# Optimization experiments

Measured on AMD Instinct MI355X. Metric: run time of the kernel, lower is better.

## Reference

```python
import jax, jax.numpy as jnp
import numpy as np

IOU_THRESHOLD = 0.1
EPS = 1e-7  # torchvision generalized_box_iou_loss eps


def _make_boxes(key, b, n, img=1000.0, wmin=10.0, wmax=120.0):
    k1, k2 = jax.random.split(key)
    cxy = jax.random.uniform(k1, (b, n, 2), jnp.float32, 0.0, img)
    wh = jax.random.uniform(k2, (b, n, 2), jnp.float32, wmin, wmax)
    return jnp.concatenate([cxy - 0.5 * wh, cxy + 0.5 * wh], axis=-1)  # xyxy


def setup_inputs() -> dict:
    key = jax.random.key(0)
    kp, kt = jax.random.split(key)
    pred_boxes = _make_boxes(kp, 16, 4096)    # [B, M, 4]
    target_boxes = _make_boxes(kt, 16, 512)   # [B, N, 4]
    return {"pred_boxes": pred_boxes, "target_boxes": target_boxes}


def _pairwise_iou(p, t):
    # p: [M,4], t: [N,4] xyxy -> [M,N]
    area_p = (p[:, 2] - p[:, 0]) * (p[:, 3] - p[:, 1])
    area_t = (t[:, 2] - t[:, 0]) * (t[:, 3] - t[:, 1])
    lt = jnp.maximum(p[:, None, :2], t[None, :, :2])
    rb = jnp.minimum(p[:, None, 2:], t[None, :, 2:])
    wh = jnp.clip(rb - lt, 0.0)
    inter = wh[..., 0] * wh[..., 1]
    union = area_p[:, None] + area_t[None, :] - inter
    return inter / union


def _greedy_match(iou):
    # Greedy: for each pred row (in order), take highest-IoU unused target with IoU > thr.
    N = iou.shape[1]
    def step(used, row):
        masked = jnp.where(used, -jnp.inf, row)  # [N]
        j = jnp.argmax(masked)
        valid = masked[j] > IOU_THRESHOLD
        used = used.at[j].set(used[j] | valid)
        return used, (j, valid)
    _, (idx, valid) = jax.lax.scan(step, jnp.zeros((N,), bool), iou)
    return idx, valid  # [M] int, [M] bool


def _giou_loss_pairs(p, t):
    # elementwise GIoU loss between p[i] and t[i]; p,t: [K,4] -> [K]
    x1 = jnp.maximum(p[:, 0], t[:, 0]); y1 = jnp.maximum(p[:, 1], t[:, 1])
    x2 = jnp.minimum(p[:, 2], t[:, 2]); y2 = jnp.minimum(p[:, 3], t[:, 3])
    inter = jnp.clip(x2 - x1, 0.0) * jnp.clip(y2 - y1, 0.0)
    area_p = (p[:, 2] - p[:, 0]) * (p[:, 3] - p[:, 1])
    area_t = (t[:, 2] - t[:, 0]) * (t[:, 3] - t[:, 1])
    union = area_p + area_t - inter
    iou = inter / (union + EPS)
    ex1 = jnp.minimum(p[:, 0], t[:, 0]); ey1 = jnp.minimum(p[:, 1], t[:, 1])
    ex2 = jnp.maximum(p[:, 2], t[:, 2]); ey2 = jnp.maximum(p[:, 3], t[:, 3])
    enc = (ex2 - ex1) * (ey2 - ey1)
    giou = iou - (enc - union) / (enc + EPS)
    return 1.0 - giou


def _image_loss(pred, tgt):
    # pred [M,4], tgt [N,4] with M != N -> greedy match then mean GIoU loss over matches
    iou = _pairwise_iou(pred, tgt)
    idx, valid = _greedy_match(iou)
    matched_t = tgt[idx]                    # [M,4]
    loss = _giou_loss_pairs(pred, matched_t)
    w = valid.astype(loss.dtype)
    cnt = w.sum()
    return jnp.where(cnt > 0, (loss * w).sum() / jnp.maximum(cnt, 1.0), 0.0)


def reference(pred_boxes, target_boxes):
    # batched path, reduction='mean': mean over per-image mean GIoU losses
    per_image = jax.vmap(_image_loss)(pred_boxes, target_boxes)  # [B]
    return per_image.mean()
```

## Files before the change

### kernel.cpp

```cpp
#include <hip/hip_runtime.h>
#include <math.h>

#define NB   16
#define NM   4096
#define NT   512
#define CAP  16
#define IOU_THR 0.1f
#define EPSG 1e-7f
#define NROWS (NB*NM)
#define T_WIN 1024
#define WROWS 2048
#define NWIN  (NM / WROWS)
#define SENT  0xFFFFFFFFu

__global__ __launch_bounds__(256) void cand_kernel(
    const float4* __restrict__ pred, const float4* __restrict__ tgt,
    int* __restrict__ counts, float2* __restrict__ cands, int* __restrict__ done_ctr)
{
    __shared__ float4 t_lds[NT];
    const int rb = blockIdx.x * 32;
    const int b  = rb >> 12;
    if (blockIdx.x == 0 && threadIdx.x == 0) *done_ctr = 0;
    #pragma unroll
    for (int i = 0; i < 2; ++i)
        t_lds[i * 256 + threadIdx.x] = tgt[b * NT + i * 256 + threadIdx.x];
    __syncthreads();

    const int wv = threadIdx.x >> 6, lane = threadIdx.x & 63;
    const int row0 = rb + wv * 8;
    const unsigned long long lmask = (1ull << lane) - 1ull;

    float4 pn0 = pred[row0],     pn1 = pred[row0 + 1];
    float4 pn2 = pred[row0 + 2], pn3 = pred[row0 + 3];
    for (int rr = 0; rr < 8; rr += 4) {
        float4 p0 = pn0, p1 = pn1, p2 = pn2, p3 = pn3;
        if (rr + 4 < 8) {
            pn0 = pred[row0 + rr + 4]; pn1 = pred[row0 + rr + 5];
            pn2 = pred[row0 + rr + 6]; pn3 = pred[row0 + rr + 7];
        }
        float ap0 = (p0.z - p0.x) * (p0.w - p0.y);
        float ap1 = (p1.z - p1.x) * (p1.w - p1.y);
        float ap2 = (p2.z - p2.x) * (p2.w - p2.y);
        float ap3 = (p3.z - p3.x) * (p3.w - p3.y);
        int base0 = 0, base1 = 0, base2 = 0, base3 = 0;
        #pragma unroll
        for (int pass = 0; pass < NT / 64; ++pass) {
            int j = (pass << 6) + lane;
            float4 t = t_lds[j];
            float at = (t.z - t.x) * (t.w - t.y);
            float w0 = fmaxf(fminf(p0.z, t.z) - fmaxf(p0.x, t.x), 0.f);
            float h0 = fmaxf(fminf(p0.w, t.w) - fmaxf(p0.y, t.y), 0.f);
            float in0 = w0 * h0;
            float iou0 = in0 * __builtin_amdgcn_rcpf((ap0 + at) - in0);
            float w1 = fmaxf(fminf(p1.z, t.z) - fmaxf(p1.x, t.x), 0.f);
            float h1 = fmaxf(fminf(p1.w, t.w) - fmaxf(p1.y, t.y), 0.f);
            float in1 = w1 * h1;
            float iou1 = in1 * __builtin_amdgcn_rcpf((ap1 + at) - in1);
            float w2 = fmaxf(fminf(p2.z, t.z) - fmaxf(p2.x, t.x), 0.f);
            float h2 = fmaxf(fminf(p2.w, t.w) - fmaxf(p2.y, t.y), 0.f);
            float in2 = w2 * h2;
            float iou2 = in2 * __builtin_amdgcn_rcpf((ap2 + at) - in2);
            float w3 = fmaxf(fminf(p3.z, t.z) - fmaxf(p3.x, t.x), 0.f);
            float h3 = fmaxf(fminf(p3.w, t.w) - fmaxf(p3.y, t.y), 0.f);
            float in3 = w3 * h3;
            float iou3 = in3 * __builtin_amdgcn_rcpf((ap3 + at) - in3);
            bool q0 = iou0 > IOU_THR, q1 = iou1 > IOU_THR;
            bool q2 = iou2 > IOU_THR, q3 = iou3 > IOU_THR;
            unsigned long long m0 = __ballot(q0), m1 = __ballot(q1);
            unsigned long long m2 = __ballot(q2), m3 = __ballot(q3);
            if (q0) {
                int off = base0 + __popcll(m0 & lmask);
                if (off < CAP)
                    cands[(size_t)off * NROWS + row0 + rr]     = make_float2(iou0, __int_as_float(j));
            }
            if (q1) {
                int off = base1 + __popcll(m1 & lmask);
                if (off < CAP)
                    cands[(size_t)off * NROWS + row0 + rr + 1] = make_float2(iou1, __int_as_float(j));
            }
            if (q2) {
                int off = base2 + __popcll(m2 & lmask);
                if (off < CAP)
                    cands[(size_t)off * NROWS + row0 + rr + 2] = make_float2(iou2, __int_as_float(j));
            }
            if (q3) {
                int off = base3 + __popcll(m3 & lmask);
                if (off < CAP)
                    cands[(size_t)off * NROWS + row0 + rr + 3] = make_float2(iou3, __int_as_float(j));
            }
            base0 += __popcll(m0); base1 += __popcll(m1);
            base2 += __popcll(m2); base3 += __popcll(m3);
        }
        if (lane == 0) {
            counts[row0 + rr]     = base0;
            counts[row0 + rr + 1] = base1;
            counts[row0 + rr + 2] = base2;
            counts[row0 + rr + 3] = base3;
        }
    }
}

__global__ __launch_bounds__(T_WIN) void win_auction(
    const float4* __restrict__ pred, const float4* __restrict__ tgt,
    const int* __restrict__ counts, const float2* __restrict__ cands,
    float* __restrict__ per_img, int* __restrict__ done_ctr,
    float* __restrict__ out)
{
    __shared__ float4   t_lds[NT];
    __shared__ unsigned claim[NT];
    __shared__ int lastprop;
    __shared__ unsigned char winovf[NWIN];
    __shared__ int ovf_min, ovf_res;
    __shared__ float rvv[T_WIN / 64];  __shared__ int rjj[T_WIN / 64];
    __shared__ float rls[T_WIN / 64];  __shared__ float rcs[T_WIN / 64];

    const int b = blockIdx.x, t = threadIdx.x, gbase = b * NM;
    const int wv = t >> 6, lane = t & 63;

    if (t < NT) {
        t_lds[t] = tgt[b * NT + t];
        claim[t] = SENT;
    }
    if (t < NWIN) winovf[t] = 0;
    if (t == 0) lastprop = -1;
    __syncthreads();

    int cw00, cw01, cw10, cw11;
    cw00 = counts[gbase + 0 * WROWS + t];
    cw01 = counts[gbase + 0 * WROWS + T_WIN + t];
    cw10 = counts[gbase + 1 * WROWS + t];
    cw11 = counts[gbase + 1 * WROWS + T_WIN + t];
    if (cw00 > CAP || cw01 > CAP) winovf[0] = 1;
    if (cw10 > CAP || cw11 > CAP) winovf[1] = 1;
    __syncthreads();

    int rglob = 0;
    #pragma unroll 1
    for (int w = 0; w < NWIN; ++w) {
        float2 c0[CAP], c1[CAP];
        #pragma unroll
        for (int e = 0; e < CAP; ++e) {
            c0[e] = cands[(size_t)e * NROWS + gbase + w * WROWS + t];
            c1[e] = cands[(size_t)e * NROWS + gbase + w * WROWS + T_WIN + t];
        }
        const unsigned row0 = (unsigned)(w * WROWS + t);
        const unsigned row1 = (unsigned)(w * WROWS + T_WIN + t);
        const int cnt0 = (w == 0) ? cw00 : cw10;
        const int cnt1 = (w == 0) ? cw01 : cw11;
        int  stt0 = (cnt0 > 0 && cnt0 <= CAP) ? 0 : 2;
        int  stt1 = (cnt1 > 0 && cnt1 <= CAP) ? 0 : 2;
        int  myj0 = -1, myj1 = -1;
        bool isovf0 = (cnt0 > CAP), isovf1 = (cnt1 > CAP);
        int  ovfj0 = -1, ovfj1 = -1;

        for (;;) {
            for (;;) {
                bool did = false;
                if (stt0 == 1 && claim[myj0] != row0) stt0 = 0;
                if (stt0 == 0) {
                    for (int it = 0; it <= CAP; ++it) {
                        float bv = -1.f; int bj = -1;
                        #pragma unroll
                        for (int e = 0; e < CAP; ++e) {
                            float2 ce = c0[e];
                            int j = __float_as_int(ce.y) & (NT - 1);
                            unsigned cj = claim[j];
                            if (e < cnt0 && cj >= row0 && ce.x > bv) { bv = ce.x; bj = j; }
                        }
                        if (bj < 0) { stt0 = 2; break; }
                        did = true;
                        unsigned old = atomicMin(&claim[bj], row0);
                        if (old >= row0) { myj0 = bj; stt0 = 1; break; }
                    }
                }
                if (stt1 == 1 && claim[myj1] != row1) stt1 = 0;
                if (stt1 == 0) {
                    for (int it = 0; it <= CAP; ++it) {
                        float bv = -1.f; int bj = -1;
                        #pragma unroll
                        for (int e = 0; e < CAP; ++e) {
                            float2 ce = c1[e];
                            int j = __float_as_int(ce.y) & (NT - 1);
                            unsigned cj = claim[j];
                            if (e < cnt1 && cj >= row1 && ce.x > bv) { bv = ce.x; bj = j; }
                        }
                        if (bj < 0) { stt1 = 2; break; }
                        did = true;
                        unsigned old = atomicMin(&claim[bj], row1);
                        if (old >= row1) { myj1 = bj; stt1 = 1; break; }
                    }
                }
                if (did) lastprop = rglob;
                __syncthreads();
                int lp = lastprop;
                ++rglob;
                if (lp < rglob - 1) break;
            }
            if (!winovf[w]) break;
            if (t == 0) ovf_min = 0x7FFFFFFF;
            __syncthreads();
            bool pend0 = isovf0 && (ovfj0 < 0 || claim[ovfj0] != row0);
            bool pend1 = isovf1 && (ovfj1 < 0 || claim[ovfj1] != row1);
            if (pend0) atomicMin(&ovf_min, (int)row0);
            if (pend1) atomicMin(&ovf_min, (int)row1);
            __syncthreads();
            const int rowF = ovf_min;
            if (rowF == 0x7FFFFFFF) break;
            {
                float4 p4 = pred[gbase + rowF];
                float v = -1.f; int bj = NT;
                if (t < NT) {
                    float4 tt = t_lds[t];
                    float area_p = (p4.z - p4.x) * (p4.w - p4.y);
                    float area_t = (tt.z - tt.x) * (tt.w - tt.y);
                    float wd = fmaxf(fminf(p4.z, tt.z) - fmaxf(p4.x, tt.x), 0.f);
                    float hd = fmaxf(fminf(p4.w, tt.w) - fmaxf(p4.y, tt.y), 0.f);
                    float inter = wd * hd;
                    float iou = inter / ((area_p + area_t) - inter);
                    bool freej = claim[t] > (unsigned)rowF;
                    v = freej ? iou : -1.f;
                    bj = freej ? t : NT;
                }
                #pragma unroll
                for (int off = 1; off < 64; off <<= 1) {
                    float ov = __shfl_xor(v, off);
                    int   oj = __shfl_xor(bj, off);
                    if (ov > v || (ov == v && oj < bj)) { v = ov; bj = oj; }
                }
                if (lane == 0) { rvv[wv] = v; rjj[wv] = bj; }
            }
            __syncthreads();
            if (t == 0) {
                float v = rvv[0]; int bj = rjj[0];
                for (int q = 1; q < T_WIN / 64; ++q)
                    if (rvv[q] > v || (rvv[q] == v && rjj[q] < bj)) { v = rvv[q]; bj = rjj[q]; }
                if (v > IOU_THR) { ovf_res = bj; claim[bj] = (unsigned)rowF; }
                else ovf_res = -1;
            }
            __syncthreads();
            if ((int)row0 == rowF) {
                if (ovf_res >= 0) ovfj0 = ovf_res;
                else isovf0 = false;
            }
            if ((int)row1 == rowF) {
                if (ovf_res >= 0) ovfj1 = ovf_res;
                else isovf1 = false;
            }
        }
    }
    __syncthreads();

    float ls = 0.f, cs = 0.f;
    if (t < NT) {
        unsigned r = claim[t];
        if (r != SENT) {
            float4 p4 = pred[gbase + (int)r];
            float4 tt = t_lds[t];
            float inter = fmaxf(fminf(p4.z, tt.z) - fmaxf(p4.x, tt.x), 0.f) *
                          fmaxf(fminf(p4.w, tt.w) - fmaxf(p4.y, tt.y), 0.f);
            float area_p = (p4.z - p4.x) * (p4.w - p4.y);
            float area_t = (tt.z - tt.x) * (tt.w - tt.y);
            float uni = area_p + area_t - inter;
            float iou = inter / (uni + EPSG);
            float enc = (fmaxf(p4.z, tt.z) - fminf(p4.x, tt.x)) *
                        (fmaxf(p4.w, tt.w) - fminf(p4.y, tt.y));
            float giou = iou - (enc - uni) / (enc + EPSG);
            ls = 1.f - giou;
            cs = 1.f;
        }
    }
    #pragma unroll
    for (int off = 32; off >= 1; off >>= 1) {
        ls += __shfl_xor(ls, off);
        cs += __shfl_xor(cs, off);
    }
    if (lane == 0) { rls[wv] = ls; rcs[wv] = cs; }
    __syncthreads();
    if (t == 0) {
        float L = 0.f, C = 0.f;
        for (int q = 0; q < T_WIN / 64; ++q) { L += rls[q]; C += rcs[q]; }
        per_img[b] = (C > 0.f) ? L / C : 0.f;
        __threadfence();
        int ret = atomicAdd(done_ctr, 1);
        if (ret == NB - 1) {
            __threadfence();
            volatile float* vp = per_img;
            float s = 0.f;
            for (int i = 0; i < NB; ++i) s += vp[i];
            out[0] = s / (float)NB;
        }
    }
}

extern "C" void kernel_launch(void* const* d_in, const int* in_sizes, int n_in,
                              void* d_out, int out_size, void* d_ws, size_t ws_size,
                              hipStream_t stream)
{
    const float4* pred = (const float4*)d_in[0];
    const float4* tgt  = (const float4*)d_in[1];

    char* ws = (char*)d_ws;
    int*    counts  = (int*)ws;
    size_t  off1    = (size_t)NROWS * sizeof(int);
    float2* cands   = (float2*)(ws + off1);
    size_t  off2    = off1 + (size_t)CAP * NROWS * sizeof(float2);
    float*  per_img = (float*)(ws + off2);
    int*    done_ctr = (int*)(ws + off2 + 64);

    cand_kernel<<<NROWS / 32, 256, 0, stream>>>(pred, tgt, counts, cands, done_ctr);
    win_auction<<<NB, T_WIN, 0, stream>>>(pred, tgt, counts, cands, per_img,
                                          done_ctr, (float*)d_out);
}
```

Measured before the change: 54.38 us.

## Fuse candidate and auction kernels with producer-consumer window flags

Merges the candidate-generation kernel and the per-image auction kernel into one launch. The first 16 blocks run the auction, and 512 producer blocks of 1024 threads compute candidates and bump per-window atomic counters that the auction blocks spin on. The aim is to overlap the auction on window 0 with candidate generation for later rows and to remove the gap between two launches. It adds a memset, spin-waiting, and a dependency on the auction blocks being resident alongside the producers; block scheduling order matters for forward progress.

```diff
diff --git a/kernel.cpp b/kernel.cpp
--- a/kernel.cpp
+++ b/kernel.cpp
@@ -8,145 +8,145 @@
 #define IOU_THR 0.1f
 #define EPSG 1e-7f
 #define NROWS (NB*NM)
-#define T_WIN 1024
+#define T_BLK 1024
 #define WROWS 2048
 #define NWIN  (NM / WROWS)
+#define NPROD 512
 #define SENT  0xFFFFFFFFu
 
-__global__ __launch_bounds__(256) void cand_kernel(
+__global__ __launch_bounds__(T_BLK) void fused_kernel(
     const float4* __restrict__ pred, const float4* __restrict__ tgt,
-    int* __restrict__ counts, float2* __restrict__ cands, int* __restrict__ done_ctr)
-{
-    __shared__ float4 t_lds[NT];
-    const int rb = blockIdx.x * 32;
-    const int b  = rb >> 12;
-    if (blockIdx.x == 0 && threadIdx.x == 0) *done_ctr = 0;
-    #pragma unroll
-    for (int i = 0; i < 2; ++i)
-        t_lds[i * 256 + threadIdx.x] = tgt[b * NT + i * 256 + threadIdx.x];
-    __syncthreads();
-
-    const int wv = threadIdx.x >> 6, lane = threadIdx.x & 63;
-    const int row0 = rb + wv * 8;
-    const unsigned long long lmask = (1ull << lane) - 1ull;
-
-    float4 pn0 = pred[row0],     pn1 = pred[row0 + 1];
-    float4 pn2 = pred[row0 + 2], pn3 = pred[row0 + 3];
-    for (int rr = 0; rr < 8; rr += 4) {
-        float4 p0 = pn0, p1 = pn1, p2 = pn2, p3 = pn3;
-        if (rr + 4 < 8) {
-            pn0 = pred[row0 + rr + 4]; pn1 = pred[row0 + rr + 5];
-            pn2 = pred[row0 + rr + 6]; pn3 = pred[row0 + rr + 7];
-        }
-        float ap0 = (p0.z - p0.x) * (p0.w - p0.y);
-        float ap1 = (p1.z - p1.x) * (p1.w - p1.y);
-        float ap2 = (p2.z - p2.x) * (p2.w - p2.y);
-        float ap3 = (p3.z - p3.x) * (p3.w - p3.y);
-        int base0 = 0, base1 = 0, base2 = 0, base3 = 0;
-        #pragma unroll
-        for (int pass = 0; pass < NT / 64; ++pass) {
-            int j = (pass << 6) + lane;
-            float4 t = t_lds[j];
-            float at = (t.z - t.x) * (t.w - t.y);
-            float w0 = fmaxf(fminf(p0.z, t.z) - fmaxf(p0.x, t.x), 0.f);
-            float h0 = fmaxf(fminf(p0.w, t.w) - fmaxf(p0.y, t.y), 0.f);
-            float in0 = w0 * h0;
-            float iou0 = in0 * __builtin_amdgcn_rcpf((ap0 + at) - in0);
-            float w1 = fmaxf(fminf(p1.z, t.z) - fmaxf(p1.x, t.x), 0.f);
-            float h1 = fmaxf(fminf(p1.w, t.w) - fmaxf(p1.y, t.y), 0.f);
-            float in1 = w1 * h1;
-            float iou1 = in1 * __builtin_amdgcn_rcpf((ap1 + at) - in1);
-            float w2 = fmaxf(fminf(p2.z, t.z) - fmaxf(p2.x, t.x), 0.f);
-            float h2 = fmaxf(fminf(p2.w, t.w) - fmaxf(p2.y, t.y), 0.f);
-            float in2 = w2 * h2;
-            float iou2 = in2 * __builtin_amdgcn_rcpf((ap2 + at) - in2);
-            float w3 = fmaxf(fminf(p3.z, t.z) - fmaxf(p3.x, t.x), 0.f);
-            float h3 = fmaxf(fminf(p3.w, t.w) - fmaxf(p3.y, t.y), 0.f);
-            float in3 = w3 * h3;
-            float iou3 = in3 * __builtin_amdgcn_rcpf((ap3 + at) - in3);
-            bool q0 = iou0 > IOU_THR, q1 = iou1 > IOU_THR;
-            bool q2 = iou2 > IOU_THR, q3 = iou3 > IOU_THR;
-            unsigned long long m0 = __ballot(q0), m1 = __ballot(q1);
-            unsigned long long m2 = __ballot(q2), m3 = __ballot(q3);
-            if (q0) {
-                int off = base0 + __popcll(m0 & lmask);
-                if (off < CAP)
-                    cands[(size_t)off * NROWS + row0 + rr]     = make_float2(iou0, __int_as_float(j));
-            }
-            if (q1) {
-                int off = base1 + __popcll(m1 & lmask);
-                if (off < CAP)
-                    cands[(size_t)off * NROWS + row0 + rr + 1] = make_float2(iou1, __int_as_float(j));
-            }
-            if (q2) {
-                int off = base2 + __popcll(m2 & lmask);
-                if (off < CAP)
-                    cands[(size_t)off * NROWS + row0 + rr + 2] = make_float2(iou2, __int_as_float(j));
-            }
-            if (q3) {
-                int off = base3 + __popcll(m3 & lmask);
-                if (off < CAP)
-                    cands[(size_t)off * NROWS + row0 + rr + 3] = make_float2(iou3, __int_as_float(j));
-            }
-            base0 += __popcll(m0); base1 += __popcll(m1);
-            base2 += __popcll(m2); base3 += __popcll(m3);
-        }
-        if (lane == 0) {
-            counts[row0 + rr]     = base0;
-            counts[row0 + rr + 1] = base1;
-            counts[row0 + rr + 2] = base2;
-            counts[row0 + rr + 3] = base3;
-        }
-    }
-}
-
-__global__ __launch_bounds__(T_WIN) void win_auction(
-    const float4* __restrict__ pred, const float4* __restrict__ tgt,
-    const int* __restrict__ counts, const float2* __restrict__ cands,
-    float* __restrict__ per_img, int* __restrict__ done_ctr,
-    float* __restrict__ out)
+    int* __restrict__ counts, float2* __restrict__ cands,
+    int* __restrict__ prod_win, float* __restrict__ per_img,
+    int* __restrict__ done_ctr, float* __restrict__ out)
 {
     __shared__ float4   t_lds[NT];
     __shared__ unsigned claim[NT];
     __shared__ int lastprop;
-    __shared__ unsigned char winovf[NWIN];
     __shared__ int ovf_min, ovf_res;
-    __shared__ float rvv[T_WIN / 64];  __shared__ int rjj[T_WIN / 64];
-    __shared__ float rls[T_WIN / 64];  __shared__ float rcs[T_WIN / 64];
-
-    const int b = blockIdx.x, t = threadIdx.x, gbase = b * NM;
+    __shared__ float rvv[T_BLK / 64];  __shared__ int rjj[T_BLK / 64];
+    __shared__ float rls[T_BLK / 64];  __shared__ float rcs[T_BLK / 64];
+
+    const int blk = blockIdx.x, t = threadIdx.x;
     const int wv = t >> 6, lane = t & 63;
 
+    if (blk >= NB) {
+        const int q  = blk - NB;
+        const int rb = q * 128;
+        const int b  = rb >> 12;
+        if (t < NT) t_lds[t] = tgt[b * NT + t];
+        __syncthreads();
+
+        const int row0 = rb + wv * 8;
+        const unsigned long long lmask = (1ull << lane) - 1ull;
+
+        float4 pn0 = pred[row0],     pn1 = pred[row0 + 1];
+        float4 pn2 = pred[row0 + 2], pn3 = pred[row0 + 3];
+        for (int rr = 0; rr < 8; rr += 4) {
+            float4 p0 = pn0, p1 = pn1, p2 = pn2, p3 = pn3;
+            if (rr + 4 < 8) {
+                pn0 = pred[row0 + rr + 4]; pn1 = pred[row0 + rr + 5];
+                pn2 = pred[row0 + rr + 6]; pn3 = pred[row0 + rr + 7];
+            }
+            float ap0 = (p0.z - p0.x) * (p0.w - p0.y);
+            float ap1 = (p1.z - p1.x) * (p1.w - p1.y);
+            float ap2 = (p2.z - p2.x) * (p2.w - p2.y);
+            float ap3 = (p3.z - p3.x) * (p3.w - p3.y);
+            int base0 = 0, base1 = 0, base2 = 0, base3 = 0;
+            #pragma unroll
+            for (int pass = 0; pass < NT / 64; ++pass) {
+                int j = (pass << 6) + lane;
+                float4 tb = t_lds[j];
+                float at = (tb.z - tb.x) * (tb.w - tb.y);
+                float w0 = fmaxf(fminf(p0.z, tb.z) - fmaxf(p0.x, tb.x), 0.f);
+                float h0 = fmaxf(fminf(p0.w, tb.w) - fmaxf(p0.y, tb.y), 0.f);
+                float in0 = w0 * h0;
+                float iou0 = in0 * __builtin_amdgcn_rcpf((ap0 + at) - in0);
+                float w1 = fmaxf(fminf(p1.z, tb.z) - fmaxf(p1.x, tb.x), 0.f);
+                float h1 = fmaxf(fminf(p1.w, tb.w) - fmaxf(p1.y, tb.y), 0.f);
+                float in1 = w1 * h1;
+                float iou1 = in1 * __builtin_amdgcn_rcpf((ap1 + at) - in1);
+                float w2 = fmaxf(fminf(p2.z, tb.z) - fmaxf(p2.x, tb.x), 0.f);
+                float h2 = fmaxf(fminf(p2.w, tb.w) - fmaxf(p2.y, tb.y), 0.f);
+                float in2 = w2 * h2;
+                float iou2 = in2 * __builtin_amdgcn_rcpf((ap2 + at) - in2);
+                float w3 = fmaxf(fminf(p3.z, tb.z) - fmaxf(p3.x, tb.x), 0.f);
+                float h3 = fmaxf(fminf(p3.w, tb.w) - fmaxf(p3.y, tb.y), 0.f);
+                float in3 = w3 * h3;
+                float iou3 = in3 * __builtin_amdgcn_rcpf((ap3 + at) - in3);
+                bool q0 = iou0 > IOU_THR, q1 = iou1 > IOU_THR;
+                bool q2 = iou2 > IOU_THR, q3 = iou3 > IOU_THR;
+                unsigned long long m0 = __ballot(q0), m1 = __ballot(q1);
+                unsigned long long m2 = __ballot(q2), m3 = __ballot(q3);
+                if (q0) {
+                    int off = base0 + __popcll(m0 & lmask);
+                    if (off < CAP)
+                        cands[(size_t)off * NROWS + row0 + rr]     = make_float2(iou0, __int_as_float(j));
+                }
+                if (q1) {
+                    int off = base1 + __popcll(m1 & lmask);
+                    if (off < CAP)
+                        cands[(size_t)off * NROWS + row0 + rr + 1] = make_float2(iou1, __int_as_float(j));
+                }
+                if (q2) {
+                    int off = base2 + __popcll(m2 & lmask);
+                    if (off < CAP)
+                        cands[(size_t)off * NROWS + row0 + rr + 2] = make_float2(iou2, __int_as_float(j));
+                }
+                if (q3) {
+                    int off = base3 + __popcll(m3 & lmask);
+                    if (off < CAP)
+                        cands[(size_t)off * NROWS + row0 + rr + 3] = make_float2(iou3, __int_as_float(j));
+                }
+                base0 += __popcll(m0); base1 += __popcll(m1);
+                base2 += __popcll(m2); base3 += __popcll(m3);
+            }
+            if (lane == 0) {
+                counts[row0 + rr]     = base0;
+                counts[row0 + rr + 1] = base1;
+                counts[row0 + rr + 2] = base2;
+                counts[row0 + rr + 3] = base3;
+            }
+        }
+        __syncthreads();
+        if (t == 0) {
+            __threadfence();
+            atomicAdd(&prod_win[q >> 4], 1);
+        }
+        return;
+    }
+
+    const int b = blk, gbase = b * NM;
     if (t < NT) {
         t_lds[t] = tgt[b * NT + t];
         claim[t] = SENT;
     }
-    if (t < NWIN) winovf[t] = 0;
     if (t == 0) lastprop = -1;
-    __syncthreads();
-
-    int cw00, cw01, cw10, cw11;
-    cw00 = counts[gbase + 0 * WROWS + t];
-    cw01 = counts[gbase + 0 * WROWS + T_WIN + t];
-    cw10 = counts[gbase + 1 * WROWS + t];
-    cw11 = counts[gbase + 1 * WROWS + T_WIN + t];
-    if (cw00 > CAP || cw01 > CAP) winovf[0] = 1;
-    if (cw10 > CAP || cw11 > CAP) winovf[1] = 1;
     __syncthreads();
 
     int rglob = 0;
     #pragma unroll 1
     for (int w = 0; w < NWIN; ++w) {
+        if (t == 0) {
+            while (__hip_atomic_load(&prod_win[b * 2 + w], __ATOMIC_ACQUIRE,
+                                     __HIP_MEMORY_SCOPE_AGENT) < 16) {}
+            __threadfence();
+        }
+        __syncthreads();
+
+        const int cnt0 = counts[gbase + w * WROWS + t];
+        const int cnt1 = counts[gbase + w * WROWS + T_BLK + t];
+        int novf = __syncthreads_count(cnt0 > CAP || cnt1 > CAP);
+        const bool haveovf = (novf > 0);
+
         float2 c0[CAP], c1[CAP];
         #pragma unroll
         for (int e = 0; e < CAP; ++e) {
             c0[e] = cands[(size_t)e * NROWS + gbase + w * WROWS + t];
-            c1[e] = cands[(size_t)e * NROWS + gbase + w * WROWS + T_WIN + t];
+            c1[e] = cands[(size_t)e * NROWS + gbase + w * WROWS + T_BLK + t];
         }
         const unsigned row0 = (unsigned)(w * WROWS + t);
-        const unsigned row1 = (unsigned)(w * WROWS + T_WIN + t);
-        const int cnt0 = (w == 0) ? cw00 : cw10;
-        const int cnt1 = (w == 0) ? cw01 : cw11;
+        const unsigned row1 = (unsigned)(w * WROWS + T_BLK + t);
         int  stt0 = (cnt0 > 0 && cnt0 <= CAP) ? 0 : 2;
         int  stt1 = (cnt1 > 0 && cnt1 <= CAP) ? 0 : 2;
         int  myj0 = -1, myj1 = -1;
@@ -196,7 +196,7 @@
                 ++rglob;
                 if (lp < rglob - 1) break;
             }
-            if (!winovf[w]) break;
+            if (!haveovf) break;
             if (t == 0) ovf_min = 0x7FFFFFFF;
             __syncthreads();
             bool pend0 = isovf0 && (ovfj0 < 0 || claim[ovfj0] != row0);
@@ -232,8 +232,8 @@
             __syncthreads();
             if (t == 0) {
                 float v = rvv[0]; int bj = rjj[0];
-                for (int q = 1; q < T_WIN / 64; ++q)
-                    if (rvv[q] > v || (rvv[q] == v && rjj[q] < bj)) { v = rvv[q]; bj = rjj[q]; }
+                for (int qq = 1; qq < T_BLK / 64; ++qq)
+                    if (rvv[qq] > v || (rvv[qq] == v && rjj[qq] < bj)) { v = rvv[qq]; bj = rjj[qq]; }
                 if (v > IOU_THR) { ovf_res = bj; claim[bj] = (unsigned)rowF; }
                 else ovf_res = -1;
             }
@@ -278,7 +278,7 @@
     __syncthreads();
     if (t == 0) {
         float L = 0.f, C = 0.f;
-        for (int q = 0; q < T_WIN / 64; ++q) { L += rls[q]; C += rcs[q]; }
+        for (int qq = 0; qq < T_BLK / 64; ++qq) { L += rls[qq]; C += rcs[qq]; }
         per_img[b] = (C > 0.f) ? L / C : 0.f;
         __threadfence();
         int ret = atomicAdd(done_ctr, 1);
@@ -305,9 +305,11 @@
     float2* cands   = (float2*)(ws + off1);
     size_t  off2    = off1 + (size_t)CAP * NROWS * sizeof(float2);
     float*  per_img = (float*)(ws + off2);
-    int*    done_ctr = (int*)(ws + off2 + 64);
-
-    cand_kernel<<<NROWS / 32, 256, 0, stream>>>(pred, tgt, counts, cands, done_ctr);
-    win_auction<<<NB, T_WIN, 0, stream>>>(pred, tgt, counts, cands, per_img,
-                                          done_ctr, (float*)d_out);
+    size_t  off3    = off2 + 128;
+    int*    done_ctr = (int*)(ws + off3);
+    int*    prod_win = done_ctr + 1;
+
+    hipMemsetAsync(done_ctr, 0, 33 * sizeof(int), stream);
+    fused_kernel<<<NB + NPROD, T_BLK, 0, stream>>>(
+        pred, tgt, counts, cands, prod_win, per_img, done_ctr, (float*)d_out);
 }
```

After: 84.72 us. 55.8% more time.
